# Kernel optimization log

Measured on AMD Instinct MI355X. Metric: run time of the kernel, lower is better.

## Reference

```python
import jax, jax.numpy as jnp
import numpy as np

D = 128      # d_model
H = 8        # n_heads
HD = D // H  # head_dim = 16
E = 256      # n_experts
R = 32       # kv_lora_rank
B, T = 4, 512
EPS = 1e-6


def _dense_init(k, fi, fo):
    s = float(1.0 / np.sqrt(fi))
    return jax.random.uniform(k, (fi, fo), minval=-s, maxval=s, dtype=jnp.float32)


def setup_inputs() -> dict:
    key = jax.random.key(0)
    ks = jax.random.split(key, 16)
    rng = np.random.RandomState(42)
    Q, _ = np.linalg.qr(rng.randn(D, D))
    glim = float(np.sqrt(6.0 / (D + D)))
    return {
        'x': jax.random.normal(ks[0], (B, T, D), dtype=jnp.float32),
        'g1': jnp.ones((D,), jnp.float32),
        'qW': _dense_init(ks[1], D, D), 'qb': jnp.zeros((D,), jnp.float32),
        'kdW': _dense_init(ks[2], D, R), 'kdb': jnp.zeros((R,), jnp.float32),
        'kuW': _dense_init(ks[3], R, 2 * D), 'kub': jnp.zeros((2 * D,), jnp.float32),
        'oW': _dense_init(ks[4], D, D), 'ob': jnp.zeros((D,), jnp.float32),
        'rot': jnp.asarray(Q, jnp.float32),
        'tq_scale': jnp.ones((D,), jnp.float32),
        's1W': _dense_init(ks[5], D, D), 's1b': jnp.zeros((D,), jnp.float32),
        's2W': _dense_init(ks[6], D, D), 's2b': jnp.zeros((D,), jnp.float32),
        'g2': jnp.ones((D,), jnp.float32),
        'gateW': _dense_init(ks[7], D, E), 'gateb': jnp.zeros((E,), jnp.float32),
        'expW': jax.random.uniform(ks[8], (E, D, D), minval=-glim, maxval=glim, dtype=jnp.float32),
        'm1W': _dense_init(ks[9], D, D), 'm1b': jnp.zeros((D,), jnp.float32),
        'm2W': _dense_init(ks[10], D, D), 'm2b': jnp.zeros((D,), jnp.float32),
    }


def _rmsnorm(x, g):
    return g * (x / jnp.sqrt(jnp.mean(x * x, axis=-1, keepdims=True) + EPS))


def _swiglu(x, w1, b1, w2, b2):
    gate = x @ w1 + b1
    return gate * jax.nn.sigmoid(gate) * (x @ w2 + b2)


def _mla(x, qW, qb, kdW, kdb, kuW, kub, oW, ob):
    b, t = x.shape[0], x.shape[1]
    q = (x @ qW + qb).reshape(b, t, H, HD)
    kv = ((x @ kdW + kdb) @ kuW + kub).reshape(b, t, H, 2 * HD)
    k, v = jnp.split(kv, 2, axis=-1)
    q = jax.nn.elu(q) + 1.0
    k = jax.nn.elu(k) + 1.0
    # linear attention: context[b,h,d,e] = sum_t k[b,t,h,d] v[b,t,h,e]
    context = jnp.einsum('bthd,bthe->bhde', k, v)
    out = jnp.einsum('bthd,bhde->bthe', q, context)
    k_sum = jnp.sum(k, axis=1)  # [b,h,d]
    z = 1.0 / (jnp.einsum('bthd,bhd->bth', q, k_sum) + EPS)
    out = out * z[..., None]
    return out.reshape(b, t, D) @ oW + ob


def _turbo_quant(x, rot, scale):
    x = x @ rot
    mag = jnp.sqrt(jnp.mean(x * x, axis=-1, keepdims=True) + EPS)
    phase = x / mag
    qp = jnp.clip(phase * 127.0, -127.0, 127.0) / 127.0
    phase = jax.lax.stop_gradient(qp - phase) + phase  # straight-through
    return phase * mag * scale


def _moe(h, gateW, gateb, expW, m1W, m1b, m2W, m2b):
    gate_scores = jax.nn.softmax(h @ gateW + gateb, axis=-1)  # [B,T,E]
    top_vals, top_idx = jax.lax.top_k(gate_scores, 2)
    top_w = top_vals / (jnp.sum(top_vals, axis=-1, keepdims=True) + EPS)
    # dense all-expert compute as in the original module
    eo = jnp.einsum('btd,edo->bteo', h, expW)  # [B,T,E,D]
    mask = jnp.sum(jax.nn.one_hot(top_idx, E, dtype=h.dtype) * top_w[..., None], axis=2)  # [B,T,E]
    wavg = jnp.einsum('bteo,bte->bto', eo, mask)
    wavg = _swiglu(wavg, m1W, m1b, m2W, m2b)
    diff_sq = jnp.square(eo - wavg[:, :, None, :])
    wvar = jnp.einsum('bteo,bte->bto', diff_sq, mask)
    consensus = jnp.exp(-jnp.mean(wvar, axis=-1))  # [B,T]
    return wavg, consensus


def reference(x, g1, qW, qb, kdW, kdb, kuW, kub, oW, ob, rot, tq_scale,
              s1W, s1b, s2W, s2b, g2, gateW, gateb, expW, m1W, m1b, m2W, m2b):
    attn_out = _turbo_quant(_mla(_rmsnorm(x, g1), qW, qb, kdW, kdb, kuW, kub, oW, ob), rot, tq_scale)
    x = x + _swiglu(attn_out, s1W, s1b, s2W, s2b)
    moe_out, consensus = _moe(_rmsnorm(x, g2), gateW, gateb, expW, m1W, m1b, m2W, m2b)
    return x + moe_out, consensus
```

## Files before the change

kernel.cpp:

```cpp
#include <hip/hip_runtime.h>
#include <math.h>

static constexpr int Dd    = 128;
static constexpr int NH    = 8;
static constexpr int NE    = 256;
static constexpr int RR    = 32;
static constexpr int TT    = 512;
static constexpr int NTOK  = 2048;
static constexpr int SLOTS = 256;
#define EPSF 1e-6f

static constexpr int FK_KV    = 0;
static constexpr int FD_CTX   = 32;
static constexpr int FD_OR    = 36;
static constexpr int FD_RG    = 37;
static constexpr int FD_ROOT  = 45;
static constexpr int FD_EXP   = 46;

__device__ __forceinline__ float elu1(float v) { return v > 0.f ? v + 1.f : expf(v); }
__device__ __forceinline__ float sigm(float v) { return 1.f / (1.f + expf(-v)); }

__device__ __forceinline__ void flag_add(int* p) {
  __hip_atomic_fetch_add(p, 1, __ATOMIC_RELEASE, __HIP_MEMORY_SCOPE_AGENT);
}
__device__ __forceinline__ void flag_wait(int* p, int tgt) {
  int c = 0;
  while (__hip_atomic_load(p, __ATOMIC_ACQUIRE, __HIP_MEMORY_SCOPE_AGENT) < tgt) {
    __builtin_amdgcn_s_sleep(2);
    if (++c > (1 << 27)) break;
  }
}

struct AParams {
  const float *x, *g1, *qW, *qb, *kdW, *kdb, *kuW, *kub, *oW, *ob, *rot, *tqs;
  const float *s1W, *s1b, *s2W, *s2b, *g2, *gateW, *gateb, *expW;
  const float *m1W, *m1b, *m2W, *m2b;
  float *kvbuf, *ctx, *ksum, *oR, *bR, *h2buf, *ybuf, *out;
  int *cnt, *slottok, *flags;
};

__global__ __launch_bounds__(512, 4) void k_all(AParams P) {
  const int tid = threadIdx.x;
  const int bid = blockIdx.x;
  const int j = tid & 127, g = tid >> 7;
  const int lane = tid & 63;
  const int n0 = bid * 4;
  const int b = bid >> 7;

  __shared__ float sh[64 * 32];
  __shared__ float4 bufA[128], bufB[128];
  __shared__ float4 part[3][128];
  __shared__ float4 gpart[256];
  __shared__ float4 rtmp[2];
  __shared__ float wvS[4][4]; __shared__ int wiS[4][4];
  __shared__ float zS[4][4];
  __shared__ int sE[4][2]; __shared__ int sSlot[4][2]; __shared__ float sWt[4][2];
  __shared__ __align__(16) float hT[128 * 20];
  __shared__ float4 y1T[128], y2T[128], inT[128], sT[128];

  float4* kpart4 = (float4*)hT;
  float4* kdT4   = (float4*)(hT + 1024);

  float xres[4];
  {
    float v[4];
    if (tid < 128) {
#pragma unroll
      for (int t = 0; t < 4; t++) { xres[t] = P.x[(n0 + t) * Dd + j]; v[t] = xres[t] * xres[t]; }
#pragma unroll
      for (int o = 32; o > 0; o >>= 1) {
#pragma unroll
        for (int t = 0; t < 4; t++) v[t] += __shfl_xor(v[t], o, 64);
      }
      if (lane == 0) rtmp[tid >> 6] = make_float4(v[0], v[1], v[2], v[3]);
    }
  }
  __syncthreads();
  if (tid < 128) {
    float g1j = P.g1[j];
#pragma unroll
    for (int t = 0; t < 4; t++) {
      float ss = ((const float*)&rtmp[0])[t] + ((const float*)&rtmp[1])[t];
      ((float*)&bufB[j])[t] = g1j * xres[t] * rsqrtf(ss * (1.f / 128.f) + EPSF);
    }
  }
  __syncthreads();

  {
    float a0 = 0, a1 = 0, a2 = 0, a3 = 0;
    const float* Wp = P.qW + (g * 32) * Dd + j;
#pragma unroll 16
    for (int i = 0; i < 32; i++) {
      float4 h4 = bufB[g * 32 + i];
      float w = Wp[i * Dd];
      a0 += h4.x * w; a1 += h4.y * w; a2 += h4.z * w; a3 += h4.w * w;
    }
    if (g) part[g - 1][j] = make_float4(a0, a1, a2, a3);
    __syncthreads();
    if (g == 0) {
      float4 p0 = part[0][j], p1 = part[1][j], p2 = part[2][j];
      float bb = P.qb[j];
      ((float*)&bufA[j])[0] = elu1(a0 + p0.x + p1.x + p2.x + bb);
      ((float*)&bufA[j])[1] = elu1(a1 + p0.y + p1.y + p2.y + bb);
      ((float*)&bufA[j])[2] = elu1(a2 + p0.z + p1.z + p2.z + bb);
      ((float*)&bufA[j])[3] = elu1(a3 + p0.w + p1.w + p2.w + bb);
    }
    __syncthreads();
  }

  if (tid < 256) {
    int col = tid & 31, ksp = tid >> 5;
    float a0 = 0, a1 = 0, a2 = 0, a3 = 0;
    const float* Wp = P.kdW + (ksp * 16) * RR + col;
#pragma unroll
    for (int i = 0; i < 16; i++) {
      float4 h4 = bufB[ksp * 16 + i];
      float w = Wp[i * RR];
      a0 += h4.x * w; a1 += h4.y * w; a2 += h4.z * w; a3 += h4.w * w;
    }
    kpart4[ksp * 32 + col] = make_float4(a0, a1, a2, a3);
  }
  __syncthreads();
  if (tid < 32) {
    float bb = P.kdb[tid];
    float s0 = bb, s1 = bb, s2 = bb, s3 = bb;
#pragma unroll
    for (int k = 0; k < 8; k++) {
      float4 p = kpart4[k * 32 + tid];
      s0 += p.x; s1 += p.y; s2 += p.z; s3 += p.w;
    }
    kdT4[tid] = make_float4(s0, s1, s2, s3);
  }
  __syncthreads();

  {
    int col = tid & 255, kh = tid >> 8;
    float a0 = 0, a1 = 0, a2 = 0, a3 = 0;
    const float* Wp = P.kuW + (kh * 16) * 256 + col;
#pragma unroll
    for (int r = 0; r < 16; r++) {
      float4 k4 = kdT4[kh * 16 + r];
      float w = Wp[r * 256];
      a0 += k4.x * w; a1 += k4.y * w; a2 += k4.z * w; a3 += k4.w * w;
    }
    if (kh) gpart[col] = make_float4(a0, a1, a2, a3);
    __syncthreads();
    if (!kh) {
      float4 p = gpart[col];
      float bb = P.kub[col];
      bool isk = (col & 31) < 16;
      float v0 = a0 + p.x + bb, v1 = a1 + p.y + bb, v2 = a2 + p.z + bb, v3 = a3 + p.w + bb;
      P.kvbuf[(n0 + 0) * 256 + col] = isk ? elu1(v0) : v0;
      P.kvbuf[(n0 + 1) * 256 + col] = isk ? elu1(v1) : v1;
      P.kvbuf[(n0 + 2) * 256 + col] = isk ? elu1(v2) : v2;
      P.kvbuf[(n0 + 3) * 256 + col] = isk ? elu1(v3) : v3;
    }
  }
  __threadfence();
  __syncthreads();
  if (tid == 0) flag_add(&P.flags[FK_KV + b * 8 + ((bid & 127) >> 4)]);

  if (bid < 256) {
    const int bh = bid >> 3, c = bid & 7;
    const int bb = bh >> 3, h = bh & 7;
    if (tid == 0) flag_wait(&P.flags[FK_KV + bb * 8 + c], 16);
    __syncthreads();
    __threadfence();
#pragma unroll
    for (int r = 0; r < 4; r++) {
      int lin = r * 512 + tid;
      int tok = lin >> 5, off = lin & 31;
      sh[lin] = P.kvbuf[((bb * TT + c * 64 + tok) * 256) + h * 32 + off];
    }
    __syncthreads();
    if (tid < 256) {
      const int d = tid >> 4, e = tid & 15;
      float acc = 0.f, ks = 0.f;
#pragma unroll 4
      for (int t = 0; t < 64; t++) {
        float kk = sh[t * 32 + d];
        acc += kk * sh[t * 32 + 16 + e];
        ks += kk;
      }
      atomicAdd(&P.ctx[bh * 256 + d * 16 + e], acc);
      if (e == 0) atomicAdd(&P.ksum[bh * 16 + d], ks);
    }
    __threadfence();
    __syncthreads();
    if (tid == 0) flag_add(&P.flags[FD_CTX + bb]);
  } else if (bid < 288) {
    int idx = (bid - 256) * 512 + tid;
    int row = idx >> 7, col = idx & 127;
    const float* ow = P.oW + row * 128;
    float acc = 0.f;
#pragma unroll 8
    for (int k = 0; k < 128; k++) acc += ow[k] * P.rot[k * 128 + col];
    P.oR[idx] = acc;
    __threadfence();
    __syncthreads();
    if (tid == 0) flag_add(&P.flags[FD_OR]);
  } else if (bid == 288) {
    if (tid < 128) {
      float acc = 0.f;
#pragma unroll 8
      for (int k = 0; k < 128; k++) acc += P.ob[k] * P.rot[k * 128 + tid];
      P.bR[tid] = acc;
    }
    __threadfence();
    __syncthreads();
    if (tid == 0) flag_add(&P.flags[FD_OR]);
  }

  if (tid == 0) flag_wait(&P.flags[FD_CTX + b], 64);
  if (tid == 1) flag_wait(&P.flags[FD_OR], 33);
  __syncthreads();
  __threadfence();

  if (tid < 128) {
    int h = j >> 4, e = j & 15;
    const float* cpt = P.ctx + (b * NH + h) * 256;
    const float* kpt = P.ksum + (b * NH + h) * 16;
    float num[4] = {0, 0, 0, 0}, den[4] = {0, 0, 0, 0};
#pragma unroll
    for (int d = 0; d < 16; d++) {
      float cx = cpt[d * 16 + e], ks = kpt[d];
      float4 q4 = bufA[h * 16 + d];
      num[0] += q4.x * cx; num[1] += q4.y * cx; num[2] += q4.z * cx; num[3] += q4.w * cx;
      den[0] += q4.x * ks; den[1] += q4.y * ks; den[2] += q4.z * ks; den[3] += q4.w * ks;
    }
#pragma unroll
    for (int t = 0; t < 4; t++) ((float*)&bufB[j])[t] = num[t] / (den[t] + EPSF);
  }
  __syncthreads();

  {
    float a0 = 0, a1 = 0, a2 = 0, a3 = 0;
    const float* Wp = P.oR + (g * 32) * Dd + j;
#pragma unroll 16
    for (int i = 0; i < 32; i++) {
      float4 h4 = bufB[g * 32 + i];
      float w = Wp[i * Dd];
      a0 += h4.x * w; a1 += h4.y * w; a2 += h4.z * w; a3 += h4.w * w;
    }
    if (g) part[g - 1][j] = make_float4(a0, a1, a2, a3);
    __syncthreads();
    float tot[4];
    if (g == 0) {
      float4 p0 = part[0][j], p1 = part[1][j], p2 = part[2][j];
      float bb = P.bR[j];
      tot[0] = a0 + p0.x + p1.x + p2.x + bb; tot[1] = a1 + p0.y + p1.y + p2.y + bb;
      tot[2] = a2 + p0.z + p1.z + p2.z + bb; tot[3] = a3 + p0.w + p1.w + p2.w + bb;
      float v[4];
#pragma unroll
      for (int t = 0; t < 4; t++) v[t] = tot[t] * tot[t];
#pragma unroll
      for (int o = 32; o > 0; o >>= 1) {
#pragma unroll
        for (int t = 0; t < 4; t++) v[t] += __shfl_xor(v[t], o, 64);
      }
      if (lane == 0) rtmp[tid >> 6] = make_float4(v[0], v[1], v[2], v[3]);
    }
    __syncthreads();
    if (g == 0) {
      float scj = P.tqs[j];
#pragma unroll
      for (int t = 0; t < 4; t++) {
        float ss = ((const float*)&rtmp[0])[t] + ((const float*)&rtmp[1])[t];
        float mag = sqrtf(ss * (1.f / 128.f) + EPSF);
        float zc = fminf(fmaxf(tot[t], -mag), mag);
        ((float*)&bufA[j])[t] = zc * scj;
      }
    }
    __syncthreads();
  }

  float xn[4] = {0.f, 0.f, 0.f, 0.f};
  {
    float a0 = 0, a1 = 0, a2 = 0, a3 = 0;
    const float* Wp = (g < 2 ? P.s1W : P.s2W) + ((g & 1) * 64) * Dd + j;
#pragma unroll 16
    for (int i = 0; i < 64; i++) {
      float4 h4 = bufA[(g & 1) * 64 + i];
      float w = Wp[i * Dd];
      a0 += h4.x * w; a1 += h4.y * w; a2 += h4.z * w; a3 += h4.w * w;
    }
    if (g) part[g - 1][j] = make_float4(a0, a1, a2, a3);
    __syncthreads();
    if (g == 0) {
      float b1 = P.s1b[j], b2 = P.s2b[j];
      float4 p0 = part[0][j], p1 = part[1][j], p2 = part[2][j];
      float gv[4], uv[4], v[4];
      gv[0] = a0 + p0.x + b1; gv[1] = a1 + p0.y + b1;
      gv[2] = a2 + p0.z + b1; gv[3] = a3 + p0.w + b1;
      uv[0] = p1.x + p2.x + b2; uv[1] = p1.y + p2.y + b2;
      uv[2] = p1.z + p2.z + b2; uv[3] = p1.w + p2.w + b2;
      float g2j = P.g2[j];
#pragma unroll
      for (int t = 0; t < 4; t++) {
        xn[t] = xres[t] + gv[t] * sigm(gv[t]) * uv[t];
        ((float*)&bufB[j])[t] = g2j * xn[t];
        v[t] = xn[t] * xn[t];
      }
#pragma unroll
      for (int o = 32; o > 0; o >>= 1) {
#pragma unroll
        for (int t = 0; t < 4; t++) v[t] += __shfl_xor(v[t], o, 64);
      }
      if (lane == 0) rtmp[tid >> 6] = make_float4(v[0], v[1], v[2], v[3]);
    }
    __syncthreads();
  }

  float val[4]; float r2v[4];
  {
    int col = tid & 255, kh = tid >> 8;
    float a0 = 0, a1 = 0, a2 = 0, a3 = 0;
    const float* Wp = P.gateW + (kh * 64) * NE + col;
#pragma unroll 16
    for (int i = 0; i < 64; i++) {
      float4 h4 = bufB[kh * 64 + i];
      float w = Wp[i * NE];
      a0 += h4.x * w; a1 += h4.y * w; a2 += h4.z * w; a3 += h4.w * w;
    }
    if (kh) gpart[col] = make_float4(a0, a1, a2, a3);
    __syncthreads();
#pragma unroll
    for (int t = 0; t < 4; t++) {
      float ss = ((const float*)&rtmp[0])[t] + ((const float*)&rtmp[1])[t];
      r2v[t] = rsqrtf(ss * (1.f / 128.f) + EPSF);
    }
    if (!kh) {
      float4 p = gpart[col];
      float bb = P.gateb[col];
      val[0] = (a0 + p.x) * r2v[0] + bb; val[1] = (a1 + p.y) * r2v[1] + bb;
      val[2] = (a2 + p.z) * r2v[2] + bb; val[3] = (a3 + p.w) * r2v[3] + bb;
    }
    if (tid < 128) {
#pragma unroll
      for (int t = 0; t < 4; t++)
        P.h2buf[(n0 + t) * Dd + j] = ((const float*)&bufB[j])[t] * r2v[t];
    }
  }
  __syncthreads();

  float m1[4]; int i1[4];
  {
    if (tid < 256) {
      float bv[4]; int bi[4];
#pragma unroll
      for (int t = 0; t < 4; t++) { bv[t] = val[t]; bi[t] = tid; }
#pragma unroll
      for (int o = 32; o > 0; o >>= 1) {
#pragma unroll
        for (int t = 0; t < 4; t++) {
          float wv = __shfl_xor(bv[t], o, 64);
          int wi = __shfl_xor(bi[t], o, 64);
          if (wv > bv[t] || (wv == bv[t] && wi < bi[t])) { bv[t] = wv; bi[t] = wi; }
        }
      }
      if (lane == 0) {
#pragma unroll
        for (int t = 0; t < 4; t++) { wvS[tid >> 6][t] = bv[t]; wiS[tid >> 6][t] = bi[t]; }
      }
    }
    __syncthreads();
    if (tid < 256) {
#pragma unroll
      for (int t = 0; t < 4; t++) {
        m1[t] = wvS[0][t]; i1[t] = wiS[0][t];
#pragma unroll
        for (int w = 1; w < 4; w++) {
          float cv = wvS[w][t]; int ci = wiS[w][t];
          if (cv > m1[t] || (cv == m1[t] && ci < i1[t])) { m1[t] = cv; i1[t] = ci; }
        }
      }
    }
    __syncthreads();
  }
  float m2[4]; int i2[4];
  {
    if (tid < 256) {
      float bv[4]; int bi[4];
#pragma unroll
      for (int t = 0; t < 4; t++) {
        bv[t] = (tid == i1[t]) ? -INFINITY : val[t];
        bi[t] = tid;
      }
#pragma unroll
      for (int o = 32; o > 0; o >>= 1) {
#pragma unroll
        for (int t = 0; t < 4; t++) {
          float wv = __shfl_xor(bv[t], o, 64);
          int wi = __shfl_xor(bi[t], o, 64);
          if (wv > bv[t] || (wv == bv[t] && wi < bi[t])) { bv[t] = wv; bi[t] = wi; }
        }
      }
      if (lane == 0) {
#pragma unroll
        for (int t = 0; t < 4; t++) { wvS[tid >> 6][t] = bv[t]; wiS[tid >> 6][t] = bi[t]; }
      }
    }
    __syncthreads();
    if (tid < 256) {
#pragma unroll
      for (int t = 0; t < 4; t++) {
        m2[t] = wvS[0][t]; i2[t] = wiS[0][t];
#pragma unroll
        for (int w = 1; w < 4; w++) {
          float cv = wvS[w][t]; int ci = wiS[w][t];
          if (cv > m2[t] || (cv == m2[t] && ci < i2[t])) { m2[t] = cv; i2[t] = ci; }
        }
      }
    }
    __syncthreads();
  }
  {
    if (tid < 256) {
      float v[4];
#pragma unroll
      for (int t = 0; t < 4; t++) v[t] = expf(val[t] - m1[t]);
#pragma unroll
      for (int o = 32; o > 0; o >>= 1) {
#pragma unroll
        for (int t = 0; t < 4; t++) v[t] += __shfl_xor(v[t], o, 64);
      }
      if (lane == 0) {
#pragma unroll
        for (int t = 0; t < 4; t++) zS[tid >> 6][t] = v[t];
      }
    }
    __syncthreads();
  }
  if (tid < 4) {
    int t = tid, tok = n0 + t;
    float Z = zS[0][t] + zS[1][t] + zS[2][t] + zS[3][t];
    float p1 = 1.f / Z;
    float p2 = expf(m2[t] - m1[t]) / Z;
    float s = p1 + p2 + EPSF;
    int e1 = i1[t], e2 = i2[t];
    int s1 = atomicAdd(&P.cnt[e1], 1); if (s1 > SLOTS - 1) s1 = SLOTS - 1;
    int s2 = atomicAdd(&P.cnt[e2], 1); if (s2 > SLOTS - 1) s2 = SLOTS - 1;
    int sl1 = e1 * SLOTS + s1, sl2 = e2 * SLOTS + s2;
    P.slottok[sl1] = tok; P.slottok[sl2] = tok;
    sE[t][0] = e1; sE[t][1] = e2;
    sSlot[t][0] = sl1; sSlot[t][1] = sl2;
    sWt[t][0] = p1 / s; sWt[t][1] = p2 / s;
  }

  __threadfence();
  __syncthreads();
  if (tid == 0) {
    int grp = bid >> 6;
    int prev = __hip_atomic_fetch_add(&P.flags[FD_RG + grp], 1,
                                      __ATOMIC_ACQ_REL, __HIP_MEMORY_SCOPE_AGENT);
    if (prev == 63) flag_add(&P.flags[FD_ROOT]);
    flag_wait(&P.flags[FD_ROOT], 8);
  }
  __syncthreads();
  __threadfence();

  {
    const int e = bid >> 1, sub = bid & 1;
    int n = __hip_atomic_load(&P.cnt[e], __ATOMIC_RELAXED, __HIP_MEMORY_SCOPE_AGENT);
    if (n > SLOTS) n = SLOTS;
    const int base = e * SLOTS;
    const float* Wp = P.expW + (size_t)e * Dd * Dd + j;
    for (int t0 = sub * 16; t0 < n; t0 += 32) {
      int m = n - t0; if (m > 16) m = 16;
      __syncthreads();
      for (int tt = g; tt < m; tt += 4) {
        int tok = P.slottok[base + t0 + tt];
        hT[j * 20 + tt] = P.h2buf[tok * Dd + j];
      }
      __syncthreads();
      float acc[4] = {0, 0, 0, 0};
#pragma unroll 8
      for (int i = 0; i < 128; i++) {
        float w = Wp[i * Dd];
        float4 h4 = *(const float4*)&hT[i * 20 + g * 4];
        acc[0] += h4.x * w; acc[1] += h4.y * w; acc[2] += h4.z * w; acc[3] += h4.w * w;
      }
#pragma unroll
      for (int k = 0; k < 4; k++) {
        int tt = g * 4 + k;
        if (tt < m) P.ybuf[(size_t)(base + t0 + tt) * Dd + j] = acc[k];
      }
    }
    __threadfence();
    __syncthreads();
    if (tid == 0) flag_add(&P.flags[FD_EXP + e]);
  }

  if (tid < 8) {
    int t = tid >> 1, sl = tid & 1;
    flag_wait(&P.flags[FD_EXP + sE[t][sl]], 2);
  }
  __syncthreads();
  __threadfence();

  {
    float y1 = P.ybuf[(size_t)sSlot[g][0] * Dd + j];
    float y2 = P.ybuf[(size_t)sSlot[g][1] * Dd + j];
    ((float*)&y1T[j])[g] = y1;
    ((float*)&y2T[j])[g] = y2;
    ((float*)&inT[j])[g] = sWt[g][0] * y1 + sWt[g][1] * y2;
  }
  __syncthreads();

  {
    float a0 = 0, a1 = 0, a2 = 0, a3 = 0;
    const float* Wp = (g < 2 ? P.m1W : P.m2W) + ((g & 1) * 64) * Dd + j;
#pragma unroll 16
    for (int i = 0; i < 64; i++) {
      float4 h4 = inT[(g & 1) * 64 + i];
      float w = Wp[i * Dd];
      a0 += h4.x * w; a1 += h4.y * w; a2 += h4.z * w; a3 += h4.w * w;
    }
    if (g) part[g - 1][j] = make_float4(a0, a1, a2, a3);
    __syncthreads();
    if (g == 0) {
      float b1 = P.m1b[j], b2 = P.m2b[j];
      float4 p0 = part[0][j], p1 = part[1][j], p2 = part[2][j];
      float gv[4], uv[4];
      gv[0] = a0 + p0.x + b1; gv[1] = a1 + p0.y + b1;
      gv[2] = a2 + p0.z + b1; gv[3] = a3 + p0.w + b1;
      uv[0] = p1.x + p2.x + b2; uv[1] = p1.y + p2.y + b2;
      uv[2] = p1.z + p2.z + b2; uv[3] = p1.w + p2.w + b2;
#pragma unroll
      for (int t = 0; t < 4; t++) {
        float sv = gv[t] * sigm(gv[t]) * uv[t];
        ((float*)&sT[j])[t] = sv;
        P.out[(n0 + t) * Dd + j] = xn[t] + sv;
      }
    }
    __syncthreads();
  }

  if (tid < 128) {
    float v[4];
#pragma unroll
    for (int t = 0; t < 4; t++) {
      float sv = ((const float*)&sT[j])[t];
      float d1 = ((const float*)&y1T[j])[t] - sv;
      float d2 = ((const float*)&y2T[j])[t] - sv;
      v[t] = sWt[t][0] * d1 * d1 + sWt[t][1] * d2 * d2;
    }
#pragma unroll
    for (int o = 32; o > 0; o >>= 1) {
#pragma unroll
      for (int t = 0; t < 4; t++) v[t] += __shfl_xor(v[t], o, 64);
    }
    if (lane == 0) rtmp[tid >> 6] = make_float4(v[0], v[1], v[2], v[3]);
  }
  __syncthreads();
  if (tid < 4) {
    float s = ((const float*)&rtmp[0])[tid] + ((const float*)&rtmp[1])[tid];
    P.out[NTOK * Dd + n0 + tid] = expf(-s * (1.f / 128.f));
  }
}

__global__ __launch_bounds__(512) void k_pre_fb(
    const float* __restrict__ x, const float* __restrict__ g1,
    const float* __restrict__ qW, const float* __restrict__ qb,
    const float* __restrict__ kdW, const float* __restrict__ kdb,
    const float* __restrict__ kuW, const float* __restrict__ kub,
    const float* __restrict__ oW, const float* __restrict__ ob,
    const float* __restrict__ rot,
    float* __restrict__ qbuf, float* __restrict__ kvbuf,
    float* __restrict__ ctx, float* __restrict__ ksum,
    int* __restrict__ cnt,
    float* __restrict__ oR, float* __restrict__ bR) {
  const int tid = threadIdx.x;
  const int bid = blockIdx.x;
  const int j = tid & 127, g = tid >> 7;
  const int lane = tid & 63;
  const int n0 = bid * 4;

  __shared__ float4 h1T[128];
  __shared__ float4 part[3][128];
  __shared__ float4 kpart[8][32];
  __shared__ float4 kdT[32];
  __shared__ float4 kupart[256];
  __shared__ float4 rtmp[2];

  if (bid == 0) {
    for (int i = tid; i < 32 * 256; i += 512) ctx[i] = 0.f;
    ksum[tid] = 0.f;
    if (tid < NE) cnt[tid] = 0;
  }

  float xv[4];
  if (tid < 128) {
    float v[4];
#pragma unroll
    for (int t = 0; t < 4; t++) { xv[t] = x[(n0 + t) * Dd + j]; v[t] = xv[t] * xv[t]; }
#pragma unroll
    for (int o = 32; o > 0; o >>= 1) {
#pragma unroll
      for (int t = 0; t < 4; t++) v[t] += __shfl_xor(v[t], o, 64);
    }
    if (lane == 0) rtmp[tid >> 6] = make_float4(v[0], v[1], v[2], v[3]);
  }
  __syncthreads();
  if (tid < 128) {
    float g1j = g1[j];
#pragma unroll
    for (int t = 0; t < 4; t++) {
      float ss = ((const float*)&rtmp[0])[t] + ((const float*)&rtmp[1])[t];
      ((float*)&h1T[j])[t] = g1j * xv[t] * rsqrtf(ss * (1.f / 128.f) + EPSF);
    }
  }
  __syncthreads();

  {
    float a0 = 0, a1 = 0, a2 = 0, a3 = 0;
    const float* Wp = qW + (g * 32) * Dd + j;
#pragma unroll 16
    for (int i = 0; i < 32; i++) {
      float4 h4 = h1T[g * 32 + i];
      float w = Wp[i * Dd];
      a0 += h4.x * w; a1 += h4.y * w; a2 += h4.z * w; a3 += h4.w * w;
    }
    if (g) part[g - 1][j] = make_float4(a0, a1, a2, a3);
    __syncthreads();
    if (g == 0) {
      float4 p0 = part[0][j], p1 = part[1][j], p2 = part[2][j];
      float bb = qb[j];
      qbuf[(n0 + 0) * Dd + j] = elu1(a0 + p0.x + p1.x + p2.x + bb);
      qbuf[(n0 + 1) * Dd + j] = elu1(a1 + p0.y + p1.y + p2.y + bb);
      qbuf[(n0 + 2) * Dd + j] = elu1(a2 + p0.z + p1.z + p2.z + bb);
      qbuf[(n0 + 3) * Dd + j] = elu1(a3 + p0.w + p1.w + p2.w + bb);
    }
    __syncthreads();
  }

  if (tid < 256) {
    int col = tid & 31, ksp = tid >> 5;
    float a0 = 0, a1 = 0, a2 = 0, a3 = 0;
    const float* Wp = kdW + (ksp * 16) * RR + col;
#pragma unroll
    for (int i = 0; i < 16; i++) {
      float4 h4 = h1T[ksp * 16 + i];
      float w = Wp[i * RR];
      a0 += h4.x * w; a1 += h4.y * w; a2 += h4.z * w; a3 += h4.w * w;
    }
    kpart[ksp][col] = make_float4(a0, a1, a2, a3);
  }
  __syncthreads();
  if (tid < 32) {
    float bb = kdb[tid];
    float s0 = bb, s1 = bb, s2 = bb, s3 = bb;
#pragma unroll
    for (int k = 0; k < 8; k++) {
      float4 p = kpart[k][tid];
      s0 += p.x; s1 += p.y; s2 += p.z; s3 += p.w;
    }
    kdT[tid] = make_float4(s0, s1, s2, s3);
  }
  __syncthreads();

  {
    int col = tid & 255, kh = tid >> 8;
    float a0 = 0, a1 = 0, a2 = 0, a3 = 0;
    const float* Wp = kuW + (kh * 16) * 256 + col;
#pragma unroll
    for (int r = 0; r < 16; r++) {
      float4 k4 = kdT[kh * 16 + r];
      float w = Wp[r * 256];
      a0 += k4.x * w; a1 += k4.y * w; a2 += k4.z * w; a3 += k4.w * w;
    }
    if (kh) kupart[col] = make_float4(a0, a1, a2, a3);
    __syncthreads();
    if (!kh) {
      float4 p = kupart[col];
      float bb = kub[col];
      bool isk = (col & 31) < 16;
      float v0 = a0 + p.x + bb, v1 = a1 + p.y + bb, v2 = a2 + p.z + bb, v3 = a3 + p.w + bb;
      kvbuf[(n0 + 0) * 256 + col] = isk ? elu1(v0) : v0;
      kvbuf[(n0 + 1) * 256 + col] = isk ? elu1(v1) : v1;
      kvbuf[(n0 + 2) * 256 + col] = isk ? elu1(v2) : v2;
      kvbuf[(n0 + 3) * 256 + col] = isk ? elu1(v3) : v3;
    }
  }

  if (bid < 32) {
    int idx = bid * 512 + tid;
    int row = idx >> 7, col = idx & 127;
    const float* ow = oW + row * 128;
    float acc = 0.f;
#pragma unroll 8
    for (int k = 0; k < 128; k++) acc += ow[k] * rot[k * 128 + col];
    oR[idx] = acc;
  } else if (bid == 32 && tid < 128) {
    float acc = 0.f;
#pragma unroll 8
    for (int k = 0; k < 128; k++) acc += ob[k] * rot[k * 128 + tid];
    bR[tid] = acc;
  }
}

__global__ __launch_bounds__(256) void k_ctx_fb(const float* __restrict__ kv,
                                                float* __restrict__ ctx,
                                                float* __restrict__ ksum) {
  const int blk = blockIdx.x;
  const int tid = threadIdx.x;
  const int bh = blk >> 3, c = blk & 7;
  const int b = bh >> 3, h = bh & 7;
  const int d = tid >> 4, e = tid & 15;
  __shared__ float sh[64 * 32];
#pragma unroll
  for (int r = 0; r < 8; r++) {
    int lin = r * 256 + tid;
    int tok = lin >> 5, off = lin & 31;
    sh[lin] = kv[((b * TT + c * 64 + tok) * 256) + h * 32 + off];
  }
  __syncthreads();
  float acc = 0.f, ks = 0.f;
#pragma unroll 4
  for (int t = 0; t < 64; t++) {
    float kk = sh[t * 32 + d];
    acc += kk * sh[t * 32 + 16 + e];
    ks += kk;
  }
  atomicAdd(&ctx[bh * 256 + d * 16 + e], acc);
  if (e == 0) atomicAdd(&ksum[bh * 16 + d], ks);
}

__global__ __launch_bounds__(512) void k_mid_fb(
    const float* __restrict__ x, const float* __restrict__ qbuf,
    const float* __restrict__ ctx, const float* __restrict__ ksum,
    const float* __restrict__ oR, const float* __restrict__ bR,
    const float* __restrict__ tqs,
    const float* __restrict__ s1W, const float* __restrict__ s1b,
    const float* __restrict__ s2W, const float* __restrict__ s2b,
    const float* __restrict__ g2, const float* __restrict__ gateW,
    const float* __restrict__ gateb,
    float* __restrict__ xnbuf, float* __restrict__ h2buf,
    float* __restrict__ gw, int* __restrict__ tokslot,
    int* __restrict__ slottok, int* __restrict__ cnt) {
  const int tid = threadIdx.x;
  const int j = tid & 127, g = tid >> 7;
  const int lane = tid & 63;
  const int n0 = blockIdx.x * 4;
  const int b = n0 >> 9;

  __shared__ float4 bufA[128], bufB[128];
  __shared__ float4 part[3][128];
  __shared__ float4 gpart[256];
  __shared__ float4 rtmp[2];
  __shared__ float wvS[4][4]; __shared__ int wiS[4][4];
  __shared__ float zS[4][4];

  float xres[4];
  if (tid < 128) {
#pragma unroll
    for (int t = 0; t < 4; t++) xres[t] = x[(n0 + t) * Dd + j];
  }
  ((float*)&bufA[j])[g] = qbuf[(n0 + g) * Dd + j];
  __syncthreads();

  if (tid < 128) {
    int h = j >> 4, e = j & 15;
    const float* cpt = ctx + (b * NH + h) * 256;
    const float* kpt = ksum + (b * NH + h) * 16;
    float num[4] = {0, 0, 0, 0}, den[4] = {0, 0, 0, 0};
#pragma unroll
    for (int d = 0; d < 16; d++) {
      float cx = cpt[d * 16 + e], ks = kpt[d];
      float4 q4 = bufA[h * 16 + d];
      num[0] += q4.x * cx; num[1] += q4.y * cx; num[2] += q4.z * cx; num[3] += q4.w * cx;
      den[0] += q4.x * ks; den[1] += q4.y * ks; den[2] += q4.z * ks; den[3] += q4.w * ks;
    }
#pragma unroll
    for (int t = 0; t < 4; t++) ((float*)&bufB[j])[t] = num[t] / (den[t] + EPSF);
  }
  __syncthreads();

  {
    float a0 = 0, a1 = 0, a2 = 0, a3 = 0;
    const float* Wp = oR + (g * 32) * Dd + j;
#pragma unroll 16
    for (int i = 0; i < 32; i++) {
      float4 h4 = bufB[g * 32 + i];
      float w = Wp[i * Dd];
      a0 += h4.x * w; a1 += h4.y * w; a2 += h4.z * w; a3 += h4.w * w;
    }
    if (g) part[g - 1][j] = make_float4(a0, a1, a2, a3);
    __syncthreads();
    float tot[4];
    if (g == 0) {
      float4 p0 = part[0][j], p1 = part[1][j], p2 = part[2][j];
      float bb = bR[j];
      tot[0] = a0 + p0.x + p1.x + p2.x + bb; tot[1] = a1 + p0.y + p1.y + p2.y + bb;
      tot[2] = a2 + p0.z + p1.z + p2.z + bb; tot[3] = a3 + p0.w + p1.w + p2.w + bb;
      float v[4];
#pragma unroll
      for (int t = 0; t < 4; t++) v[t] = tot[t] * tot[t];
#pragma unroll
      for (int o = 32; o > 0; o >>= 1) {
#pragma unroll
        for (int t = 0; t < 4; t++) v[t] += __shfl_xor(v[t], o, 64);
      }
      if (lane == 0) rtmp[tid >> 6] = make_float4(v[0], v[1], v[2], v[3]);
    }
    __syncthreads();
    if (g == 0) {
      float scj = tqs[j];
#pragma unroll
      for (int t = 0; t < 4; t++) {
        float ss = ((const float*)&rtmp[0])[t] + ((const float*)&rtmp[1])[t];
        float mag = sqrtf(ss * (1.f / 128.f) + EPSF);
        float zc = fminf(fmaxf(tot[t], -mag), mag);
        ((float*)&bufA[j])[t] = zc * scj;
      }
    }
    __syncthreads();
  }

  {
    float a0 = 0, a1 = 0, a2 = 0, a3 = 0;
    const float* Wp = (g < 2 ? s1W : s2W) + ((g & 1) * 64) * Dd + j;
#pragma unroll 16
    for (int i = 0; i < 64; i++) {
      float4 h4 = bufA[(g & 1) * 64 + i];
      float w = Wp[i * Dd];
      a0 += h4.x * w; a1 += h4.y * w; a2 += h4.z * w; a3 += h4.w * w;
    }
    if (g) part[g - 1][j] = make_float4(a0, a1, a2, a3);
    __syncthreads();
    if (g == 0) {
      float b1 = s1b[j], b2 = s2b[j];
      float4 p0 = part[0][j], p1 = part[1][j], p2 = part[2][j];
      float gv[4], uv[4], xn[4], v[4];
      gv[0] = a0 + p0.x + b1; gv[1] = a1 + p0.y + b1;
      gv[2] = a2 + p0.z + b1; gv[3] = a3 + p0.w + b1;
      uv[0] = p1.x + p2.x + b2; uv[1] = p1.y + p2.y + b2;
      uv[2] = p1.z + p2.z + b2; uv[3] = p1.w + p2.w + b2;
      float g2j = g2[j];
#pragma unroll
      for (int t = 0; t < 4; t++) {
        xn[t] = xres[t] + gv[t] * sigm(gv[t]) * uv[t];
        xnbuf[(n0 + t) * Dd + j] = xn[t];
        ((float*)&bufB[j])[t] = g2j * xn[t];
        v[t] = xn[t] * xn[t];
      }
#pragma unroll
      for (int o = 32; o > 0; o >>= 1) {
#pragma unroll
        for (int t = 0; t < 4; t++) v[t] += __shfl_xor(v[t], o, 64);
      }
      if (lane == 0) rtmp[tid >> 6] = make_float4(v[0], v[1], v[2], v[3]);
    }
    __syncthreads();
// ... 340 lines not shown
```

Baseline: 163.3 us.

## Map threads to token-column pairs instead of k-split partial sums in fused kernel

Thread groups now each own one token and one output column, so the q, o-projection, SwiGLU and MoE-MLP matvecs run over the full K=128 per thread. This removes the shared-memory partial-sum buffers and the extra reduction barriers. The kv-up and gate matvecs now use 256 threads over the full K instead of splitting K across two halves. Each thread now reads four times as many weights from global/L2, and half the block sits idle in some phases, in exchange for fewer syncs and less LDS traffic.

```diff
diff --git a/kernel.cpp b/kernel.cpp
--- a/kernel.cpp
+++ b/kernel.cpp
@@ -42,15 +42,16 @@
 __global__ __launch_bounds__(512, 4) void k_all(AParams P) {
   const int tid = threadIdx.x;
   const int bid = blockIdx.x;
-  const int j = tid & 127, g = tid >> 7;
+  const int t  = tid >> 7;
+  const int j2 = tid & 127;
   const int lane = tid & 63;
   const int n0 = bid * 4;
   const int b = bid >> 7;
 
   __shared__ float sh[64 * 32];
-  __shared__ float4 bufA[128], bufB[128];
-  __shared__ float4 part[3][128];
-  __shared__ float4 gpart[256];
+  __shared__ float4 bufA[128];
+  __shared__ float4 bufB[128];
+  __shared__ float ws1[8], ws2[8];
   __shared__ float4 rtmp[2];
   __shared__ float wvS[4][4]; __shared__ int wiS[4][4];
   __shared__ float zS[4][4];
@@ -61,51 +62,26 @@
   float4* kpart4 = (float4*)hT;
   float4* kdT4   = (float4*)(hT + 1024);
 
-  float xres[4];
-  {
-    float v[4];
-    if (tid < 128) {
-#pragma unroll
-      for (int t = 0; t < 4; t++) { xres[t] = P.x[(n0 + t) * Dd + j]; v[t] = xres[t] * xres[t]; }
-#pragma unroll
-      for (int o = 32; o > 0; o >>= 1) {
-#pragma unroll
-        for (int t = 0; t < 4; t++) v[t] += __shfl_xor(v[t], o, 64);
-      }
-      if (lane == 0) rtmp[tid >> 6] = make_float4(v[0], v[1], v[2], v[3]);
-    }
-  }
-  __syncthreads();
-  if (tid < 128) {
-    float g1j = P.g1[j];
-#pragma unroll
-    for (int t = 0; t < 4; t++) {
-      float ss = ((const float*)&rtmp[0])[t] + ((const float*)&rtmp[1])[t];
-      ((float*)&bufB[j])[t] = g1j * xres[t] * rsqrtf(ss * (1.f / 128.f) + EPSF);
-    }
-  }
-  __syncthreads();
-
-  {
-    float a0 = 0, a1 = 0, a2 = 0, a3 = 0;
-    const float* Wp = P.qW + (g * 32) * Dd + j;
-#pragma unroll 16
-    for (int i = 0; i < 32; i++) {
-      float4 h4 = bufB[g * 32 + i];
-      float w = Wp[i * Dd];
-      a0 += h4.x * w; a1 += h4.y * w; a2 += h4.z * w; a3 += h4.w * w;
-    }
-    if (g) part[g - 1][j] = make_float4(a0, a1, a2, a3);
-    __syncthreads();
-    if (g == 0) {
-      float4 p0 = part[0][j], p1 = part[1][j], p2 = part[2][j];
-      float bb = P.qb[j];
-      ((float*)&bufA[j])[0] = elu1(a0 + p0.x + p1.x + p2.x + bb);
-      ((float*)&bufA[j])[1] = elu1(a1 + p0.y + p1.y + p2.y + bb);
-      ((float*)&bufA[j])[2] = elu1(a2 + p0.z + p1.z + p2.z + bb);
-      ((float*)&bufA[j])[3] = elu1(a3 + p0.w + p1.w + p2.w + bb);
-    }
-    __syncthreads();
+  const float xv_s = P.x[(n0 + t) * Dd + j2];
+  {
+    float v = xv_s * xv_s;
+#pragma unroll
+    for (int o = 32; o > 0; o >>= 1) v += __shfl_xor(v, o, 64);
+    if (lane == 0) ws1[tid >> 6] = v;
+  }
+  __syncthreads();
+  {
+    float ss = ws1[2 * t] + ws1[2 * t + 1];
+    ((float*)&bufB[j2])[t] = P.g1[j2] * xv_s * rsqrtf(ss * (1.f / 128.f) + EPSF);
+  }
+  __syncthreads();
+
+  {
+    float acc = 0.f;
+    const float* Wp = P.qW + j2;
+#pragma unroll 8
+    for (int i = 0; i < 128; i++) acc += ((const float*)&bufB[i])[t] * Wp[i * Dd];
+    ((float*)&bufA[j2])[t] = elu1(acc + P.qb[j2]);
   }
 
   if (tid < 256) {
@@ -133,28 +109,23 @@
   }
   __syncthreads();
 
-  {
-    int col = tid & 255, kh = tid >> 8;
+  if (tid < 256) {
+    const int col = tid;
     float a0 = 0, a1 = 0, a2 = 0, a3 = 0;
-    const float* Wp = P.kuW + (kh * 16) * 256 + col;
-#pragma unroll
-    for (int r = 0; r < 16; r++) {
-      float4 k4 = kdT4[kh * 16 + r];
+    const float* Wp = P.kuW + col;
+#pragma unroll
+    for (int r = 0; r < 32; r++) {
+      float4 k4 = kdT4[r];
       float w = Wp[r * 256];
       a0 += k4.x * w; a1 += k4.y * w; a2 += k4.z * w; a3 += k4.w * w;
     }
-    if (kh) gpart[col] = make_float4(a0, a1, a2, a3);
-    __syncthreads();
-    if (!kh) {
-      float4 p = gpart[col];
-      float bb = P.kub[col];
-      bool isk = (col & 31) < 16;
-      float v0 = a0 + p.x + bb, v1 = a1 + p.y + bb, v2 = a2 + p.z + bb, v3 = a3 + p.w + bb;
-      P.kvbuf[(n0 + 0) * 256 + col] = isk ? elu1(v0) : v0;
-      P.kvbuf[(n0 + 1) * 256 + col] = isk ? elu1(v1) : v1;
-      P.kvbuf[(n0 + 2) * 256 + col] = isk ? elu1(v2) : v2;
-      P.kvbuf[(n0 + 3) * 256 + col] = isk ? elu1(v3) : v3;
-    }
+    float bb = P.kub[col];
+    bool isk = (col & 31) < 16;
+    float v0 = a0 + bb, v1 = a1 + bb, v2 = a2 + bb, v3 = a3 + bb;
+    P.kvbuf[(n0 + 0) * 256 + col] = isk ? elu1(v0) : v0;
+    P.kvbuf[(n0 + 1) * 256 + col] = isk ? elu1(v1) : v1;
+    P.kvbuf[(n0 + 2) * 256 + col] = isk ? elu1(v2) : v2;
+    P.kvbuf[(n0 + 3) * 256 + col] = isk ? elu1(v3) : v3;
   }
   __threadfence();
   __syncthreads();
@@ -177,9 +148,9 @@
       const int d = tid >> 4, e = tid & 15;
       float acc = 0.f, ks = 0.f;
 #pragma unroll 4
-      for (int t = 0; t < 64; t++) {
-        float kk = sh[t * 32 + d];
-        acc += kk * sh[t * 32 + 16 + e];
+      for (int tk = 0; tk < 64; tk++) {
+        float kk = sh[tk * 32 + d];
+        acc += kk * sh[tk * 32 + 16 + e];
         ks += kk;
       }
       atomicAdd(&P.ctx[bh * 256 + d * 16 + e], acc);
@@ -217,7 +188,7 @@
   __threadfence();
 
   if (tid < 128) {
-    int h = j >> 4, e = j & 15;
+    int h = j2 >> 4, e = j2 & 15;
     const float* cpt = P.ctx + (b * NH + h) * 256;
     const float* kpt = P.ksum + (b * NH + h) * 16;
     float num[4] = {0, 0, 0, 0}, den[4] = {0, 0, 0, 0};
@@ -229,117 +200,69 @@
       den[0] += q4.x * ks; den[1] += q4.y * ks; den[2] += q4.z * ks; den[3] += q4.w * ks;
     }
 #pragma unroll
-    for (int t = 0; t < 4; t++) ((float*)&bufB[j])[t] = num[t] / (den[t] + EPSF);
-  }
-  __syncthreads();
-
-  {
-    float a0 = 0, a1 = 0, a2 = 0, a3 = 0;
-    const float* Wp = P.oR + (g * 32) * Dd + j;
-#pragma unroll 16
-    for (int i = 0; i < 32; i++) {
-      float4 h4 = bufB[g * 32 + i];
-      float w = Wp[i * Dd];
-      a0 += h4.x * w; a1 += h4.y * w; a2 += h4.z * w; a3 += h4.w * w;
-    }
-    if (g) part[g - 1][j] = make_float4(a0, a1, a2, a3);
-    __syncthreads();
-    float tot[4];
-    if (g == 0) {
-      float4 p0 = part[0][j], p1 = part[1][j], p2 = part[2][j];
-      float bb = P.bR[j];
-      tot[0] = a0 + p0.x + p1.x + p2.x + bb; tot[1] = a1 + p0.y + p1.y + p2.y + bb;
-      tot[2] = a2 + p0.z + p1.z + p2.z + bb; tot[3] = a3 + p0.w + p1.w + p2.w + bb;
-      float v[4];
-#pragma unroll
-      for (int t = 0; t < 4; t++) v[t] = tot[t] * tot[t];
-#pragma unroll
-      for (int o = 32; o > 0; o >>= 1) {
-#pragma unroll
-        for (int t = 0; t < 4; t++) v[t] += __shfl_xor(v[t], o, 64);
-      }
-      if (lane == 0) rtmp[tid >> 6] = make_float4(v[0], v[1], v[2], v[3]);
-    }
-    __syncthreads();
-    if (g == 0) {
-      float scj = P.tqs[j];
-#pragma unroll
-      for (int t = 0; t < 4; t++) {
-        float ss = ((const float*)&rtmp[0])[t] + ((const float*)&rtmp[1])[t];
-        float mag = sqrtf(ss * (1.f / 128.f) + EPSF);
-        float zc = fminf(fmaxf(tot[t], -mag), mag);
-        ((float*)&bufA[j])[t] = zc * scj;
-      }
-    }
-    __syncthreads();
-  }
-
-  float xn[4] = {0.f, 0.f, 0.f, 0.f};
-  {
-    float a0 = 0, a1 = 0, a2 = 0, a3 = 0;
-    const float* Wp = (g < 2 ? P.s1W : P.s2W) + ((g & 1) * 64) * Dd + j;
-#pragma unroll 16
-    for (int i = 0; i < 64; i++) {
-      float4 h4 = bufA[(g & 1) * 64 + i];
-      float w = Wp[i * Dd];
-      a0 += h4.x * w; a1 += h4.y * w; a2 += h4.z * w; a3 += h4.w * w;
-    }
-    if (g) part[g - 1][j] = make_float4(a0, a1, a2, a3);
-    __syncthreads();
-    if (g == 0) {
-      float b1 = P.s1b[j], b2 = P.s2b[j];
-      float4 p0 = part[0][j], p1 = part[1][j], p2 = part[2][j];
-      float gv[4], uv[4], v[4];
-      gv[0] = a0 + p0.x + b1; gv[1] = a1 + p0.y + b1;
-      gv[2] = a2 + p0.z + b1; gv[3] = a3 + p0.w + b1;
-      uv[0] = p1.x + p2.x + b2; uv[1] = p1.y + p2.y + b2;
-      uv[2] = p1.z + p2.z + b2; uv[3] = p1.w + p2.w + b2;
-      float g2j = P.g2[j];
-#pragma unroll
-      for (int t = 0; t < 4; t++) {
-        xn[t] = xres[t] + gv[t] * sigm(gv[t]) * uv[t];
-        ((float*)&bufB[j])[t] = g2j * xn[t];
-        v[t] = xn[t] * xn[t];
-      }
-#pragma unroll
-      for (int o = 32; o > 0; o >>= 1) {
-#pragma unroll
-        for (int t = 0; t < 4; t++) v[t] += __shfl_xor(v[t], o, 64);
-      }
-      if (lane == 0) rtmp[tid >> 6] = make_float4(v[0], v[1], v[2], v[3]);
-    }
-    __syncthreads();
-  }
+    for (int tt = 0; tt < 4; tt++) ((float*)&bufB[j2])[tt] = num[tt] / (den[tt] + EPSF);
+  }
+  __syncthreads();
+
+  {
+    float acc = 0.f;
+    const float* Wp = P.oR + j2;
+#pragma unroll 8
+    for (int i = 0; i < 128; i++) acc += ((const float*)&bufB[i])[t] * Wp[i * Dd];
+    float tot = acc + P.bR[j2];
+    float v = tot * tot;
+#pragma unroll
+    for (int o = 32; o > 0; o >>= 1) v += __shfl_xor(v, o, 64);
+    if (lane == 0) ws1[tid >> 6] = v;
+    __syncthreads();
+    float ss = ws1[2 * t] + ws1[2 * t + 1];
+    float mag = sqrtf(ss * (1.f / 128.f) + EPSF);
+    float zc = fminf(fmaxf(tot, -mag), mag);
+    ((float*)&bufA[j2])[t] = zc * P.tqs[j2];
+  }
+  __syncthreads();
+
+  float xn_s;
+  {
+    float a1 = 0.f, a2 = 0.f;
+    const float* W1 = P.s1W + j2;
+    const float* W2 = P.s2W + j2;
+#pragma unroll 8
+    for (int i = 0; i < 128; i++) {
+      float h = ((const float*)&bufA[i])[t];
+      a1 += h * W1[i * Dd];
+      a2 += h * W2[i * Dd];
+    }
+    float gv = a1 + P.s1b[j2], uv = a2 + P.s2b[j2];
+    xn_s = xv_s + gv * sigm(gv) * uv;
+    float v = xn_s * xn_s;
+#pragma unroll
+    for (int o = 32; o > 0; o >>= 1) v += __shfl_xor(v, o, 64);
+    if (lane == 0) ws2[tid >> 6] = v;
+    ((float*)&bufB[j2])[t] = P.g2[j2] * xn_s;
+  }
+  __syncthreads();
 
   float val[4]; float r2v[4];
   {
-    int col = tid & 255, kh = tid >> 8;
-    float a0 = 0, a1 = 0, a2 = 0, a3 = 0;
-    const float* Wp = P.gateW + (kh * 64) * NE + col;
-#pragma unroll 16
-    for (int i = 0; i < 64; i++) {
-      float4 h4 = bufB[kh * 64 + i];
-      float w = Wp[i * NE];
-      a0 += h4.x * w; a1 += h4.y * w; a2 += h4.z * w; a3 += h4.w * w;
-    }
-    if (kh) gpart[col] = make_float4(a0, a1, a2, a3);
-    __syncthreads();
-#pragma unroll
-    for (int t = 0; t < 4; t++) {
-      float ss = ((const float*)&rtmp[0])[t] + ((const float*)&rtmp[1])[t];
-      r2v[t] = rsqrtf(ss * (1.f / 128.f) + EPSF);
-    }
-    if (!kh) {
-      float4 p = gpart[col];
+#pragma unroll
+    for (int tt = 0; tt < 4; tt++)
+      r2v[tt] = rsqrtf((ws2[2 * tt] + ws2[2 * tt + 1]) * (1.f / 128.f) + EPSF);
+    if (tid < 256) {
+      const int col = tid;
+      float a[4] = {0, 0, 0, 0};
+      const float* Wp = P.gateW + col;
+#pragma unroll 4
+      for (int i = 0; i < 128; i++) {
+        float4 h4 = bufB[i];
+        float w = Wp[i * NE];
+        a[0] += h4.x * w; a[1] += h4.y * w; a[2] += h4.z * w; a[3] += h4.w * w;
+      }
       float bb = P.gateb[col];
-      val[0] = (a0 + p.x) * r2v[0] + bb; val[1] = (a1 + p.y) * r2v[1] + bb;
-      val[2] = (a2 + p.z) * r2v[2] + bb; val[3] = (a3 + p.w) * r2v[3] + bb;
-    }
-    if (tid < 128) {
-#pragma unroll
-      for (int t = 0; t < 4; t++)
-        P.h2buf[(n0 + t) * Dd + j] = ((const float*)&bufB[j])[t] * r2v[t];
-    }
+#pragma unroll
+      for (int tt = 0; tt < 4; tt++) val[tt] = a[tt] * r2v[tt] + bb;
+    }
+    P.h2buf[(n0 + t) * Dd + j2] = P.g2[j2] * xn_s * r2v[t];
   }
   __syncthreads();
 
@@ -348,30 +271,30 @@
     if (tid < 256) {
       float bv[4]; int bi[4];
 #pragma unroll
-      for (int t = 0; t < 4; t++) { bv[t] = val[t]; bi[t] = tid; }
+      for (int tt = 0; tt < 4; tt++) { bv[tt] = val[tt]; bi[tt] = tid; }
 #pragma unroll
       for (int o = 32; o > 0; o >>= 1) {
 #pragma unroll
-        for (int t = 0; t < 4; t++) {
-          float wv = __shfl_xor(bv[t], o, 64);
-          int wi = __shfl_xor(bi[t], o, 64);
-          if (wv > bv[t] || (wv == bv[t] && wi < bi[t])) { bv[t] = wv; bi[t] = wi; }
+        for (int tt = 0; tt < 4; tt++) {
+          float wv = __shfl_xor(bv[tt], o, 64);
+          int wi = __shfl_xor(bi[tt], o, 64);
+          if (wv > bv[tt] || (wv == bv[tt] && wi < bi[tt])) { bv[tt] = wv; bi[tt] = wi; }
         }
       }
       if (lane == 0) {
 #pragma unroll
-        for (int t = 0; t < 4; t++) { wvS[tid >> 6][t] = bv[t]; wiS[tid >> 6][t] = bi[t]; }
+        for (int tt = 0; tt < 4; tt++) { wvS[tid >> 6][tt] = bv[tt]; wiS[tid >> 6][tt] = bi[tt]; }
       }
     }
     __syncthreads();
     if (tid < 256) {
 #pragma unroll
-      for (int t = 0; t < 4; t++) {
-        m1[t] = wvS[0][t]; i1[t] = wiS[0][t];
+      for (int tt = 0; tt < 4; tt++) {
+        m1[tt] = wvS[0][tt]; i1[tt] = wiS[0][tt];
 #pragma unroll
         for (int w = 1; w < 4; w++) {
-          float cv = wvS[w][t]; int ci = wiS[w][t];
-          if (cv > m1[t] || (cv == m1[t] && ci < i1[t])) { m1[t] = cv; i1[t] = ci; }
+          float cv = wvS[w][tt]; int ci = wiS[w][tt];
+          if (cv > m1[tt] || (cv == m1[tt] && ci < i1[tt])) { m1[tt] = cv; i1[tt] = ci; }
         }
       }
     }
@@ -382,33 +305,33 @@
     if (tid < 256) {
       float bv[4]; int bi[4];
 #pragma unroll
-      for (int t = 0; t < 4; t++) {
-        bv[t] = (tid == i1[t]) ? -INFINITY : val[t];
-        bi[t] = tid;
+      for (int tt = 0; tt < 4; tt++) {
+        bv[tt] = (tid == i1[tt]) ? -INFINITY : val[tt];
+        bi[tt] = tid;
       }
 #pragma unroll
       for (int o = 32; o > 0; o >>= 1) {
 #pragma unroll
-        for (int t = 0; t < 4; t++) {
-          float wv = __shfl_xor(bv[t], o, 64);
-          int wi = __shfl_xor(bi[t], o, 64);
-          if (wv > bv[t] || (wv == bv[t] && wi < bi[t])) { bv[t] = wv; bi[t] = wi; }
+        for (int tt = 0; tt < 4; tt++) {
+          float wv = __shfl_xor(bv[tt], o, 64);
+          int wi = __shfl_xor(bi[tt], o, 64);
+          if (wv > bv[tt] || (wv == bv[tt] && wi < bi[tt])) { bv[tt] = wv; bi[tt] = wi; }
         }
       }
       if (lane == 0) {
 #pragma unroll
-        for (int t = 0; t < 4; t++) { wvS[tid >> 6][t] = bv[t]; wiS[tid >> 6][t] = bi[t]; }
+        for (int tt = 0; tt < 4; tt++) { wvS[tid >> 6][tt] = bv[tt]; wiS[tid >> 6][tt] = bi[tt]; }
       }
     }
     __syncthreads();
     if (tid < 256) {
 #pragma unroll
-      for (int t = 0; t < 4; t++) {
-        m2[t] = wvS[0][t]; i2[t] = wiS[0][t];
+      for (int tt = 0; tt < 4; tt++) {
+        m2[tt] = wvS[0][tt]; i2[tt] = wiS[0][tt];
 #pragma unroll
         for (int w = 1; w < 4; w++) {
-          float cv = wvS[w][t]; int ci = wiS[w][t];
-          if (cv > m2[t] || (cv == m2[t] && ci < i2[t])) { m2[t] = cv; i2[t] = ci; }
+          float cv = wvS[w][tt]; int ci = wiS[w][tt];
+          if (cv > m2[tt] || (cv == m2[tt] && ci < i2[tt])) { m2[tt] = cv; i2[tt] = ci; }
         }
       }
     }
@@ -418,33 +341,33 @@
     if (tid < 256) {
       float v[4];
 #pragma unroll
-      for (int t = 0; t < 4; t++) v[t] = expf(val[t] - m1[t]);
+      for (int tt = 0; tt < 4; tt++) v[tt] = expf(val[tt] - m1[tt]);
 #pragma unroll
       for (int o = 32; o > 0; o >>= 1) {
 #pragma unroll
-        for (int t = 0; t < 4; t++) v[t] += __shfl_xor(v[t], o, 64);
+        for (int tt = 0; tt < 4; tt++) v[tt] += __shfl_xor(v[tt], o, 64);
       }
       if (lane == 0) {
 #pragma unroll
-        for (int t = 0; t < 4; t++) zS[tid >> 6][t] = v[t];
+        for (int tt = 0; tt < 4; tt++) zS[tid >> 6][tt] = v[tt];
       }
     }
     __syncthreads();
   }
   if (tid < 4) {
-    int t = tid, tok = n0 + t;
-    float Z = zS[0][t] + zS[1][t] + zS[2][t] + zS[3][t];
+    int tt = tid, tok = n0 + tt;
+    float Z = zS[0][tt] + zS[1][tt] + zS[2][tt] + zS[3][tt];
     float p1 = 1.f / Z;
-    float p2 = expf(m2[t] - m1[t]) / Z;
+    float p2 = expf(m2[tt] - m1[tt]) / Z;
     float s = p1 + p2 + EPSF;
-    int e1 = i1[t], e2 = i2[t];
+    int e1 = i1[tt], e2 = i2[tt];
     int s1 = atomicAdd(&P.cnt[e1], 1); if (s1 > SLOTS - 1) s1 = SLOTS - 1;
     int s2 = atomicAdd(&P.cnt[e2], 1); if (s2 > SLOTS - 1) s2 = SLOTS - 1;
     int sl1 = e1 * SLOTS + s1, sl2 = e2 * SLOTS + s2;
     P.slottok[sl1] = tok; P.slottok[sl2] = tok;
-    sE[t][0] = e1; sE[t][1] = e2;
-    sSlot[t][0] = sl1; sSlot[t][1] = sl2;
-    sWt[t][0] = p1 / s; sWt[t][1] = p2 / s;
+    sE[tt][0] = e1; sE[tt][1] = e2;
+    sSlot[tt][0] = sl1; sSlot[tt][1] = sl2;
+    sWt[tt][0] = p1 / s; sWt[tt][1] = p2 / s;
   }
 
   __threadfence();
@@ -464,26 +387,26 @@
     int n = __hip_atomic_load(&P.cnt[e], __ATOMIC_RELAXED, __HIP_MEMORY_SCOPE_AGENT);
     if (n > SLOTS) n = SLOTS;
     const int base = e * SLOTS;
-    const float* Wp = P.expW + (size_t)e * Dd * Dd + j;
+    const float* Wp = P.expW + (size_t)e * Dd * Dd + j2;
     for (int t0 = sub * 16; t0 < n; t0 += 32) {
       int m = n - t0; if (m > 16) m = 16;
       __syncthreads();
-      for (int tt = g; tt < m; tt += 4) {
+      for (int tt = t; tt < m; tt += 4) {
         int tok = P.slottok[base + t0 + tt];
-        hT[j * 20 + tt] = P.h2buf[tok * Dd + j];
+        hT[j2 * 20 + tt] = P.h2buf[tok * Dd + j2];
       }
       __syncthreads();
       float acc[4] = {0, 0, 0, 0};
 #pragma unroll 8
       for (int i = 0; i < 128; i++) {
         float w = Wp[i * Dd];
-        float4 h4 = *(const float4*)&hT[i * 20 + g * 4];
+        float4 h4 = *(const float4*)&hT[i * 20 + t * 4];
         acc[0] += h4.x * w; acc[1] += h4.y * w; acc[2] += h4.z * w; acc[3] += h4.w * w;
       }
 #pragma unroll
       for (int k = 0; k < 4; k++) {
-        int tt = g * 4 + k;
-        if (tt < m) P.ybuf[(size_t)(base + t0 + tt) * Dd + j] = acc[k];
+        int tt = t * 4 + k;
+        if (tt < m) P.ybuf[(size_t)(base + t0 + tt) * Dd + j2] = acc[k];
       }
     }
     __threadfence();
@@ -492,63 +415,51 @@
   }
 
   if (tid < 8) {
-    int t = tid >> 1, sl = tid & 1;
-    flag_wait(&P.flags[FD_EXP + sE[t][sl]], 2);
+    int tt = tid >> 1, sl = tid & 1;
+    flag_wait(&P.flags[FD_EXP + sE[tt][sl]], 2);
   }
   __syncthreads();
   __threadfence();
 
   {
-    float y1 = P.ybuf[(size_t)sSlot[g][0] * Dd + j];
-    float y2 = P.ybuf[(size_t)sSlot[g][1] * Dd + j];
-    ((float*)&y1T[j])[g] = y1;
-    ((float*)&y2T[j])[g] = y2;
-    ((float*)&inT[j])[g] = sWt[g][0] * y1 + sWt[g][1] * y2;
-  }
-  __syncthreads();
-
-  {
-    float a0 = 0, a1 = 0, a2 = 0, a3 = 0;
-    const float* Wp = (g < 2 ? P.m1W : P.m2W) + ((g & 1) * 64) * Dd + j;
-#pragma unroll 16
-    for (int i = 0; i < 64; i++) {
-      float4 h4 = inT[(g & 1) * 64 + i];
-      float w = Wp[i * Dd];
-      a0 += h4.x * w; a1 += h4.y * w; a2 += h4.z * w; a3 += h4.w * w;
-    }
-    if (g) part[g - 1][j] = make_float4(a0, a1, a2, a3);
-    __syncthreads();
-    if (g == 0) {
-      float b1 = P.m1b[j], b2 = P.m2b[j];
-      float4 p0 = part[0][j], p1 = part[1][j], p2 = part[2][j];
-      float gv[4], uv[4];
-      gv[0] = a0 + p0.x + b1; gv[1] = a1 + p0.y + b1;
-      gv[2] = a2 + p0.z + b1; gv[3] = a3 + p0.w + b1;
-      uv[0] = p1.x + p2.x + b2; uv[1] = p1.y + p2.y + b2;
-      uv[2] = p1.z + p2.z + b2; uv[3] = p1.w + p2.w + b2;
-#pragma unroll
-      for (int t = 0; t < 4; t++) {
-        float sv = gv[t] * sigm(gv[t]) * uv[t];
-        ((float*)&sT[j])[t] = sv;
-        P.out[(n0 + t) * Dd + j] = xn[t] + sv;
-      }
-    }
-    __syncthreads();
-  }
+    float y1 = P.ybuf[(size_t)sSlot[t][0] * Dd + j2];
+    float y2 = P.ybuf[(size_t)sSlot[t][1] * Dd + j2];
+    ((float*)&y1T[j2])[t] = y1;
+    ((float*)&y2T[j2])[t] = y2;
+    ((float*)&inT[j2])[t] = sWt[t][0] * y1 + sWt[t][1] * y2;
+  }
+  __syncthreads();
+
+  {
+    float a1 = 0.f, a2 = 0.f;
+    const float* W1 = P.m1W + j2;
+    const float* W2 = P.m2W + j2;
+#pragma unroll 8
+    for (int i = 0; i < 128; i++) {
+      float h = ((const float*)&inT[i])[t];
+      a1 += h * W1[i * Dd];
+      a2 += h * W2[i * Dd];
+    }
+    float gv = a1 + P.m1b[j2], uv = a2 + P.m2b[j2];
+    float sv = gv * sigm(gv) * uv;
+    ((float*)&sT[j2])[t] = sv;
+    P.out[(n0 + t) * Dd + j2] = xn_s + sv;
+  }
+  __syncthreads();
 
   if (tid < 128) {
     float v[4];
 #pragma unroll
-    for (int t = 0; t < 4; t++) {
-      float sv = ((const float*)&sT[j])[t];
-      float d1 = ((const float*)&y1T[j])[t] - sv;
-      float d2 = ((const float*)&y2T[j])[t] - sv;
-      v[t] = sWt[t][0] * d1 * d1 + sWt[t][1] * d2 * d2;
+    for (int tt = 0; tt < 4; tt++) {
+      float sv = ((const float*)&sT[j2])[tt];
+      float d1 = ((const float*)&y1T[j2])[tt] - sv;
+      float d2 = ((const float*)&y2T[j2])[tt] - sv;
+      v[tt] = sWt[tt][0] * d1 * d1 + sWt[tt][1] * d2 * d2;
     }
 #pragma unroll
     for (int o = 32; o > 0; o >>= 1) {
 #pragma unroll
-      for (int t = 0; t < 4; t++) v[t] += __shfl_xor(v[t], o, 64);
+      for (int tt = 0; tt < 4; tt++) v[tt] += __shfl_xor(v[tt], o, 64);
     }
     if (lane == 0) rtmp[tid >> 6] = make_float4(v[0], v[1], v[2], v[3]);
   }
```

Result: no change. 164.5 us (+0.8%).
